# Kernel optimization log

Hardware: AMD Instinct MI355X
Metric: run time of the kernel (lower is better)

The kernel has to match this reference:

```python
import jax, jax.numpy as jnp
import numpy as np

D_MODEL = 256
N_HEADS = 8
KEY_DIM = 256  # keras code passes key_dim=d_model
DFF = 1024
B, T, S = 8, 1024, 1024
LN_EPS = 1e-3  # keras LayerNormalization default epsilon
NEG = -1e9


def _mha(q_in, kv_in, Wq, bq, Wk, bk, Wv, bv, Wo, bo, causal):
    # q/k/v: [b, t, n, h]
    q = jnp.einsum('btd,dnh->btnh', q_in, Wq) + bq
    k = jnp.einsum('bsd,dnh->bsnh', kv_in, Wk) + bk
    v = jnp.einsum('bsd,dnh->bsnh', kv_in, Wv) + bv
    scale = 1.0 / jnp.sqrt(jnp.asarray(KEY_DIM, q.dtype))
    scores = jnp.einsum('btnh,bsnh->bnts', q * scale, k)  # [b,n,t,s]
    if causal:
        mask = jnp.tril(jnp.ones((q_in.shape[1], kv_in.shape[1]), dtype=bool))
        scores = jnp.where(mask, scores, NEG)
    attn = jax.nn.softmax(scores, axis=-1)
    out = jnp.einsum('bnts,bsnh->btnh', attn, v)
    return jnp.einsum('btnh,nhd->btd', out, Wo) + bo, attn


def _layernorm(x, gamma, beta):
    mu = jnp.mean(x, axis=-1, keepdims=True)
    var = jnp.var(x, axis=-1, keepdims=True)
    return (x - mu) * jax.lax.rsqrt(var + LN_EPS) * gamma + beta


def setup_inputs() -> dict:
    key = jax.random.key(0)
    ks = jax.random.split(key, 24)
    s = 0.02
    def n(k, shape):
        return jax.random.normal(k, shape, dtype=jnp.float32) * s
    inp = {
        'x': jax.random.normal(ks[0], (B, T, D_MODEL), dtype=jnp.float32),
        'context': jax.random.normal(ks[1], (B, S, D_MODEL), dtype=jnp.float32),
        # causal self-attention MHA params
        'Wq1': n(ks[2], (D_MODEL, N_HEADS, KEY_DIM)), 'bq1': jnp.zeros((N_HEADS, KEY_DIM), jnp.float32),
        'Wk1': n(ks[3], (D_MODEL, N_HEADS, KEY_DIM)), 'bk1': jnp.zeros((N_HEADS, KEY_DIM), jnp.float32),
        'Wv1': n(ks[4], (D_MODEL, N_HEADS, KEY_DIM)), 'bv1': jnp.zeros((N_HEADS, KEY_DIM), jnp.float32),
        'Wo1': n(ks[5], (N_HEADS, KEY_DIM, D_MODEL)), 'bo1': jnp.zeros((D_MODEL,), jnp.float32),
        'g1': jnp.ones((D_MODEL,), jnp.float32), 'be1': jnp.zeros((D_MODEL,), jnp.float32),
        # cross-attention MHA params
        'Wq2': n(ks[6], (D_MODEL, N_HEADS, KEY_DIM)), 'bq2': jnp.zeros((N_HEADS, KEY_DIM), jnp.float32),
        'Wk2': n(ks[7], (D_MODEL, N_HEADS, KEY_DIM)), 'bk2': jnp.zeros((N_HEADS, KEY_DIM), jnp.float32),
        'Wv2': n(ks[8], (D_MODEL, N_HEADS, KEY_DIM)), 'bv2': jnp.zeros((N_HEADS, KEY_DIM), jnp.float32),
        'Wo2': n(ks[9], (N_HEADS, KEY_DIM, D_MODEL)), 'bo2': jnp.zeros((D_MODEL,), jnp.float32),
        'g2': jnp.ones((D_MODEL,), jnp.float32), 'be2': jnp.zeros((D_MODEL,), jnp.float32),
        # FFN params
        'W1': n(ks[10], (D_MODEL, DFF)), 'b1': jnp.zeros((DFF,), jnp.float32),
        'W2': n(ks[11], (DFF, D_MODEL)), 'b2': jnp.zeros((D_MODEL,), jnp.float32),
        'g3': jnp.ones((D_MODEL,), jnp.float32), 'be3': jnp.zeros((D_MODEL,), jnp.float32),
    }
    return inp


def reference(x, context,
              Wq1, bq1, Wk1, bk1, Wv1, bv1, Wo1, bo1, g1, be1,
              Wq2, bq2, Wk2, bk2, Wv2, bv2, Wo2, bo2, g2, be2,
              W1, b1, W2, b2, g3, be3):
    # causal self-attention + add&norm
    attn_out, _ = _mha(x, x, Wq1, bq1, Wk1, bk1, Wv1, bv1, Wo1, bo1, causal=True)
    x = _layernorm(x + attn_out, g1, be1)
    # cross-attention + add&norm
    attn_out, _ = _mha(x, context, Wq2, bq2, Wk2, bk2, Wv2, bv2, Wo2, bo2, causal=False)
    x = _layernorm(x + attn_out, g2, be2)
    # FFN (dropout is identity at inference) + add&norm
    h = jax.nn.relu(jnp.einsum('btd,df->btf', x, W1) + b1)
    ff = jnp.einsum('btf,fd->btd', h, W2) + b2
    x = _layernorm(x + ff, g3, be3)
    return x
```

## Files before the change

kernel.cpp:

```cpp
#include <hip/hip_runtime.h>
#include <hip/hip_bf16.h>
#include <math.h>

#define BATCH   8
#define SEQ     1024
#define DMODEL  256
#define NHEADS  8
#define HDIM    256
#define NQKV    2048
#define DFF     1024
#define MROWS   (BATCH*SEQ)
#define LN_EPS  1e-3f
#define ATT_SCALE 0.0625f

typedef unsigned int  uint;
typedef unsigned short ushort;
typedef __attribute__((ext_vector_type(8))) __bf16 bf16x8;
typedef __attribute__((ext_vector_type(4))) float   f32x4;
typedef __attribute__((ext_vector_type(4))) ushort  ushort4v;

__device__ __forceinline__ float b2f(ushort h) {
    union { uint u; float f; } v; v.u = ((uint)h) << 16; return v.f;
}
__device__ __forceinline__ ushort f2b(float f) {
    union { float f; uint u; } v; v.f = f;
    return (ushort)((v.u + 0x7FFFu + ((v.u >> 16) & 1u)) >> 16);
}
__device__ __forceinline__ uint pk2(float a, float b) {
    return (uint)f2b(a) | ((uint)f2b(b) << 16);
}

template<int EPI, int OUTBF>
__global__ __launch_bounds__(256, 2)
void gemm_bf16(const ushort* __restrict__ A, const ushort* __restrict__ Bt,
               const float* __restrict__ bias, const float* __restrict__ resid,
               void* __restrict__ Cv, int K, int lda, int ldc)
{
    __shared__ ushort As[128 * 64];
    __shared__ ushort Bs[128 * 64];
    const int t  = threadIdx.x;
    const int l  = t & 63;
    const int w  = t >> 6;
    const int wm = w >> 1, wn = w & 1;
    const int m0 = blockIdx.y * 128, n0 = blockIdx.x * 128;
    const int lg = l >> 4, lr = l & 15;

    f32x4 acc[4][4];
    #pragma unroll
    for (int i = 0; i < 4; i++)
        #pragma unroll
        for (int j = 0; j < 4; j++)
            acc[i][j] = (f32x4){0.f, 0.f, 0.f, 0.f};

    for (int k0 = 0; k0 < K; k0 += 64) {
        uint4 av[4], bv[4];
        #pragma unroll
        for (int j = 0; j < 4; j++) {
            const int chunk = t + j * 256;
            const int row   = chunk >> 3;
            const int ce    = (chunk & 7) * 8;
            av[j] = *(const uint4*)&A [(size_t)(m0 + row) * lda + k0 + ce];
            bv[j] = *(const uint4*)&Bt[(size_t)(n0 + row) * K   + k0 + ce];
        }
        __syncthreads();
        #pragma unroll
        for (int j = 0; j < 4; j++) {
            const int chunk = t + j * 256;
            const int row   = chunk >> 3;
            const int woff  = (chunk * 16) ^ ((row & 7) << 4);
            *(uint4*)((char*)As + woff) = av[j];
            *(uint4*)((char*)Bs + woff) = bv[j];
        }
        __syncthreads();
        #pragma unroll
        for (int c = 0; c < 2; c++) {
            bf16x8 af[4], bf[4];
            #pragma unroll
            for (int i = 0; i < 4; i++) {
                const int rowA = wm * 64 + i * 16 + lr;
                const int offA = (rowA * 128 + c * 64 + lg * 16) ^ ((rowA & 7) << 4);
                af[i] = *(const bf16x8*)((const char*)As + offA);
                const int rowB = wn * 64 + i * 16 + lr;
                const int offB = (rowB * 128 + c * 64 + lg * 16) ^ ((rowB & 7) << 4);
                bf[i] = *(const bf16x8*)((const char*)Bs + offB);
            }
            #pragma unroll
            for (int mi = 0; mi < 4; mi++)
                #pragma unroll
                for (int ni = 0; ni < 4; ni++)
                    acc[mi][ni] = __builtin_amdgcn_mfma_f32_16x16x32_bf16(
                        af[mi], bf[ni], acc[mi][ni], 0, 0, 0);
        }
    }

    #pragma unroll
    for (int ni = 0; ni < 4; ni++) {
        const int col = n0 + wn * 64 + ni * 16 + lr;
        const float bb = bias[col];
        #pragma unroll
        for (int mi = 0; mi < 4; mi++) {
            #pragma unroll
            for (int r = 0; r < 4; r++) {
                const int row = m0 + wm * 64 + mi * 16 + lg * 4 + r;
                float v = acc[mi][ni][r] + bb;
                if (EPI == 1) v = fmaxf(v, 0.f);
                if (EPI == 2) v += resid[(size_t)row * ldc + col];
                if (OUTBF) ((ushort*)Cv)[(size_t)row * ldc + col] = f2b(v);
                else       ((float*) Cv)[(size_t)row * ldc + col] = v;
            }
        }
    }
}

__global__ __launch_bounds__(256)
void vtrans(const ushort* __restrict__ V, ushort* __restrict__ Vt)
{
    __shared__ ushort tl[64][72];
    const int s0 = blockIdx.x * 64;
    const int d0 = blockIdx.y * 64;
    const int bh = blockIdx.z;
    const int b  = bh >> 3, h = bh & 7;
    const int t  = threadIdx.x;
    #pragma unroll
    for (int j = 0; j < 2; j++) {
        const int chunk = t + j * 256;
        const int row = chunk >> 3, c8 = (chunk & 7) * 8;
        *(uint4*)&tl[row][c8] =
            *(const uint4*)&V[((size_t)(b * SEQ + s0 + row)) * NQKV + h * HDIM + d0 + c8];
    }
    __syncthreads();
    #pragma unroll
    for (int j = 0; j < 2; j++) {
        const int chunk = t + j * 256;
        const int dr = chunk >> 3, s8 = (chunk & 7) * 8;
        ushort tmp[8] __attribute__((aligned(16)));
        #pragma unroll
        for (int i = 0; i < 8; i++) tmp[i] = tl[s8 + i][dr];
        *(uint4*)&Vt[((size_t)(bh * HDIM + d0 + dr)) * SEQ + s0 + s8] = *(const uint4*)tmp;
    }
}

template<bool CAUSAL>
__global__ __launch_bounds__(256, 1)
void attn_mfma(const ushort* __restrict__ Q, const ushort* __restrict__ K,
               const ushort* __restrict__ Vt, ushort* __restrict__ O)
{
    __shared__ __align__(16) char lds[37888];

    const int t  = threadIdx.x;
    const int w  = t >> 6, l = t & 63;
    const int lg = l >> 4, lr = l & 15;
    const int orig = blockIdx.x + (blockIdx.y << 4) + (blockIdx.z << 7);
    const int lin  = ((orig & 7) << 7) + (orig >> 3);
    const int qt0  = (lin & 15) << 6;
    const int h    = (lin >> 4) & 7;
    const int b    = lin >> 7;

    const size_t qgbase = ((size_t)(b * SEQ + qt0)) * NQKV + (size_t)h * HDIM;
    #pragma unroll
    for (int j = 0; j < 8; j++) {
        const int chunk = t + j * 256;
        const int row = chunk >> 5, slot = chunk & 31;
        const uint4 v = *(const uint4*)&Q[qgbase + (size_t)row * NQKV + slot * 8];
        *(uint4*)(lds + row * 512 + ((slot * 16) ^ ((row & 7) << 4))) = v;
    }

    const size_t kgbase = (size_t)b * SEQ * NQKV + (size_t)h * HDIM;
    const size_t vgbase = ((size_t)(b * NHEADS + h)) * HDIM * SEQ;
    const int ntiles = CAUSAL ? (qt0 / 32 + 2) : (SEQ / 32);

    uint4 kv[4], vv[4];
    #pragma unroll
    for (int j = 0; j < 4; j++) {
        const int chunk = t + j * 256;
        const int krow = chunk >> 5, kslot = chunk & 31;
        kv[j] = *(const uint4*)&K[kgbase + (size_t)krow * NQKV + kslot * 8];
        const int vrow = chunk >> 2, vslot = chunk & 3;
        vv[j] = *(const uint4*)&Vt[vgbase + (size_t)vrow * SEQ + vslot * 8];
    }

    __syncthreads();
    bf16x8 qa[8];
    {
        const int qrow = w * 16 + lr;
        const int sw = (qrow & 7) << 4;
        #pragma unroll
        for (int ks = 0; ks < 8; ks++)
            qa[ks] = *(const bf16x8*)(lds + qrow * 512 + ((lg * 16 + ks * 64) ^ sw));
    }

    f32x4 oacc[16];
    #pragma unroll
    for (int i = 0; i < 16; i++) oacc[i] = (f32x4){0.f, 0.f, 0.f, 0.f};
    float m_[4], l_[4];
    #pragma unroll
    for (int r = 0; r < 4; r++) { m_[r] = -INFINITY; l_[r] = 0.f; }

    ushort* Pw = (ushort*)(lds + 32768 + w * 1280);

    for (int tile = 0; tile < ntiles; tile++) {
        const int s0 = tile * 32;
        __syncthreads();
        #pragma unroll
        for (int j = 0; j < 4; j++) {
            const int chunk = t + j * 256;
            const int krow = chunk >> 5, kslot = chunk & 31;
            *(uint4*)(lds + krow * 512 + ((kslot * 16) ^ ((krow & 7) << 4))) = kv[j];
            const int vrow = chunk >> 2, vslot = chunk & 3;
            *(uint4*)(lds + 16384 + vrow * 64 + ((vslot * 16) ^ ((vrow & 3) << 4))) = vv[j];
        }
        __syncthreads();

        if (tile + 1 < ntiles) {
            const int s0n = s0 + 32;
            #pragma unroll
            for (int j = 0; j < 4; j++) {
                const int chunk = t + j * 256;
                const int krow = chunk >> 5, kslot = chunk & 31;
                kv[j] = *(const uint4*)&K[kgbase + (size_t)(s0n + krow) * NQKV + kslot * 8];
                const int vrow = chunk >> 2, vslot = chunk & 3;
                vv[j] = *(const uint4*)&Vt[vgbase + (size_t)vrow * SEQ + s0n + vslot * 8];
            }
        }

        f32x4 sacc[2];
        sacc[0] = (f32x4){0.f, 0.f, 0.f, 0.f};
        sacc[1] = (f32x4){0.f, 0.f, 0.f, 0.f};
        #pragma unroll
        for (int ks = 0; ks < 8; ks++) {
            #pragma unroll
            for (int st = 0; st < 2; st++) {
                const int srow = st * 16 + lr;
                const bf16x8 kb = *(const bf16x8*)(lds + srow * 512 +
                                   ((lg * 16 + ks * 64) ^ ((srow & 7) << 4)));
                sacc[st] = __builtin_amdgcn_mfma_f32_16x16x32_bf16(qa[ks], kb, sacc[st], 0, 0, 0);
            }
        }

        const bool maskq = CAUSAL && (s0 + 31 > qt0 + w * 16);
        float e0[4], e1[4], corr[4];
        #pragma unroll
        for (int r = 0; r < 4; r++) {
            float p0 = sacc[0][r] * ATT_SCALE;
            float p1 = sacc[1][r] * ATT_SCALE;
            if (maskq) {
                const int qg = qt0 + w * 16 + lg * 4 + r;
                if (s0 + lr > qg)      p0 = -1e9f;
                if (s0 + 16 + lr > qg) p1 = -1e9f;
            }
            float mx = fmaxf(p0, p1);
            mx = fmaxf(mx, __shfl_xor(mx, 1));
            mx = fmaxf(mx, __shfl_xor(mx, 2));
            mx = fmaxf(mx, __shfl_xor(mx, 4));
            mx = fmaxf(mx, __shfl_xor(mx, 8));
            const float newm = fmaxf(m_[r], mx);
            corr[r] = __expf(m_[r] - newm);
            m_[r] = newm;
            e0[r] = __expf(p0 - newm);
            e1[r] = __expf(p1 - newm);
            float es = e0[r] + e1[r];
            es += __shfl_xor(es, 1);
            es += __shfl_xor(es, 2);
            es += __shfl_xor(es, 4);
            es += __shfl_xor(es, 8);
            l_[r] = l_[r] * corr[r] + es;
        }
        #pragma unroll
        for (int r = 0; r < 4; r++) {
            Pw[(lg * 4 + r) * 40 + lr]      = f2b(e0[r]);
            Pw[(lg * 4 + r) * 40 + 16 + lr] = f2b(e1[r]);
        }
        #pragma unroll
        for (int dt = 0; dt < 16; dt++) {
            oacc[dt][0] *= corr[0]; oacc[dt][1] *= corr[1];
            oacc[dt][2] *= corr[2]; oacc[dt][3] *= corr[3];
        }

        const bf16x8 pa = *(const bf16x8*)((const char*)Pw + lr * 80 + lg * 16);
        #pragma unroll
        for (int dt = 0; dt < 16; dt++) {
            const int vrow = dt * 16 + lr;
            const bf16x8 vb = *(const bf16x8*)(lds + 16384 + vrow * 64 +
                               ((lg * 16) ^ ((vrow & 3) << 4)));
            oacc[dt] = __builtin_amdgcn_mfma_f32_16x16x32_bf16(pa, vb, oacc[dt], 0, 0, 0);
        }
    }

    float inv[4];
    #pragma unroll
    for (int r = 0; r < 4; r++) inv[r] = 1.f / l_[r];
    const size_t obase = ((size_t)(b * SEQ + qt0 + w * 16)) * NQKV + (size_t)h * HDIM;
    #pragma unroll
    for (int dt = 0; dt < 16; dt++) {
        #pragma unroll
        for (int r = 0; r < 4; r++) {
            O[obase + (size_t)(lg * 4 + r) * NQKV + dt * 16 + lr] =
                f2b(oacc[dt][r] * inv[r]);
        }
    }
}

__global__ __launch_bounds__(256)
void ln_f32(const float* __restrict__ X, const float* __restrict__ gamma,
            const float* __restrict__ beta, float* __restrict__ Y,
            ushort* __restrict__ Yb)
{
    const int lane = threadIdx.x & 63;
    const int row  = blockIdx.x * 4 + (threadIdx.x >> 6);
    const float4 v = *(const float4*)&X[(size_t)row * DMODEL + lane * 4];
    float s = v.x + v.y + v.z + v.w;
    #pragma unroll
    for (int o = 1; o < 64; o <<= 1) s += __shfl_xor(s, o);
    const float mu = s * (1.f / 256.f);
    const float dx = v.x - mu, dy = v.y - mu, dz = v.z - mu, dw = v.w - mu;
    float ss = dx*dx + dy*dy + dz*dz + dw*dw;
    #pragma unroll
    for (int o = 1; o < 64; o <<= 1) ss += __shfl_xor(ss, o);
    const float rstd = rsqrtf(ss * (1.f / 256.f) + LN_EPS);
    const float4 gv = *(const float4*)&gamma[lane * 4];
    const float4 bv = *(const float4*)&beta[lane * 4];
    float4 out;
    out.x = dx * rstd * gv.x + bv.x;
    out.y = dy * rstd * gv.y + bv.y;
    out.z = dz * rstd * gv.z + bv.z;
    out.w = dw * rstd * gv.w + bv.w;
    *(float4*)&Y[(size_t)row * DMODEL + lane * 4] = out;
    if (Yb) {
        uint2 p; p.x = pk2(out.x, out.y); p.y = pk2(out.z, out.w);
        *(uint2*)&Yb[(size_t)row * DMODEL + lane * 4] = p;
    }
}

__global__ __launch_bounds__(256)
void cast_f2b(const float* __restrict__ X, ushort* __restrict__ Y, int n8)
{
    const int i = blockIdx.x * 256 + threadIdx.x;
    if (i < n8) {
        const float4 a = *(const float4*)&X[(size_t)i * 8];
        const float4 b = *(const float4*)&X[(size_t)i * 8 + 4];
        uint4 o;
        o.x = pk2(a.x, a.y); o.y = pk2(a.z, a.w);
        o.z = pk2(b.x, b.y); o.w = pk2(b.z, b.w);
        *(uint4*)&Y[(size_t)i * 8] = o;
    }
}

__global__ __launch_bounds__(256)
void castT_f2b(const float* __restrict__ W, ushort* __restrict__ Wt, int Kd, int Nd)
{
    __shared__ float tile[32][33];
    const int k0 = blockIdx.y * 32, n0 = blockIdx.x * 32;
    const int r  = threadIdx.x >> 3;
    const int c4 = (threadIdx.x & 7) * 4;
    const float4 v = *(const float4*)&W[(size_t)(k0 + r) * Nd + n0 + c4];
    tile[r][c4+0] = v.x; tile[r][c4+1] = v.y; tile[r][c4+2] = v.z; tile[r][c4+3] = v.w;
    __syncthreads();
    ushort4v ov = { f2b(tile[c4+0][r]), f2b(tile[c4+1][r]),
                    f2b(tile[c4+2][r]), f2b(tile[c4+3][r]) };
    *(ushort4v*)&Wt[(size_t)(n0 + r) * Kd + k0 + c4] = ov;
}

extern "C" void kernel_launch(void* const* d_in, const int* in_sizes, int n_in,
                              void* d_out, int out_size, void* d_ws, size_t ws_size,
                              hipStream_t stream)
{
    const float* x    = (const float*)d_in[0];
    const float* ctx  = (const float*)d_in[1];
    const float* Wq1  = (const float*)d_in[2];
    const float* bq1  = (const float*)d_in[3];
    const float* Wk1  = (const float*)d_in[4];
    const float* bk1  = (const float*)d_in[5];
    const float* Wv1  = (const float*)d_in[6];
    const float* bv1  = (const float*)d_in[7];
    const float* Wo1  = (const float*)d_in[8];
    const float* bo1  = (const float*)d_in[9];
    const float* g1   = (const float*)d_in[10];
    const float* be1  = (const float*)d_in[11];
    const float* Wq2  = (const float*)d_in[12];
    const float* bq2  = (const float*)d_in[13];
    const float* Wk2  = (const float*)d_in[14];
    const float* bk2  = (const float*)d_in[15];
    const float* Wv2  = (const float*)d_in[16];
    const float* bv2  = (const float*)d_in[17];
    const float* Wo2  = (const float*)d_in[18];
    const float* bo2  = (const float*)d_in[19];
    const float* g2   = (const float*)d_in[20];
    const float* be2  = (const float*)d_in[21];
    const float* W1   = (const float*)d_in[22];
    const float* b1   = (const float*)d_in[23];
    const float* W2   = (const float*)d_in[24];
    const float* b2   = (const float*)d_in[25];
    const float* g3   = (const float*)d_in[26];
    const float* be3  = (const float*)d_in[27];
    (void)in_sizes; (void)n_in; (void)out_size; (void)ws_size;

    char* base = (char*)d_ws;
    const size_t MB1 = 1024 * 1024;
    ushort* Qb   = (ushort*)(base + 0 * MB1);
    ushort* Kb   = (ushort*)(base + 32 * MB1);
    ushort* Vb   = (ushort*)(base + 64 * MB1);
    float*  Yf   = (float*) (base + 96 * MB1);
    float*  X1f  = (float*) (base + 104 * MB1);
    float*  X2f  = (float*) (base + 112 * MB1);
    ushort* xb   = (ushort*)(base + 120 * MB1);
    ushort* ctxb = (ushort*)(base + 124 * MB1);
    ushort* X1b  = (ushort*)(base + 128 * MB1);
    ushort* X2b  = (ushort*)(base + 132 * MB1);
    ushort* wq1t = (ushort*)(base + 136 * MB1);
    ushort* wk1t = (ushort*)(base + 137 * MB1);
    ushort* wv1t = (ushort*)(base + 138 * MB1);
    ushort* wo1t = (ushort*)(base + 139 * MB1);
    ushort* wq2t = (ushort*)(base + 140 * MB1);
    ushort* wk2t = (ushort*)(base + 141 * MB1);
    ushort* wv2t = (ushort*)(base + 142 * MB1);
    ushort* wo2t = (ushort*)(base + 143 * MB1);
    ushort* w1t  = (ushort*)(base + 144 * MB1);
    ushort* w2t  = (ushort*)(base + 144 * MB1 + 512 * 1024);
    ushort* Hb   = (ushort*)(base + 145 * MB1);
    ushort* Vtg  = (ushort*)(base + 161 * MB1);

    const dim3 blk(256);
    const dim3 gQKV(NQKV/128, MROWS/128);
    const dim3 gOut(DMODEL/128, MROWS/128);
    const dim3 gF1(DFF/128, MROWS/128);
    const dim3 gAttn(SEQ/64, NHEADS, BATCH);
    const dim3 gVT(SEQ/64, HDIM/64, BATCH*NHEADS);
    const dim3 gLN(MROWS/4);

    cast_f2b<<<dim3((MROWS*DMODEL/8 + 255)/256), blk, 0, stream>>>(x,   xb,   MROWS*DMODEL/8);
    cast_f2b<<<dim3((MROWS*DMODEL/8 + 255)/256), blk, 0, stream>>>(ctx, ctxb, MROWS*DMODEL/8);
    castT_f2b<<<dim3(NQKV/32, DMODEL/32), blk, 0, stream>>>(Wq1, wq1t, DMODEL, NQKV);
    castT_f2b<<<dim3(NQKV/32, DMODEL/32), blk, 0, stream>>>(Wk1, wk1t, DMODEL, NQKV);
    castT_f2b<<<dim3(NQKV/32, DMODEL/32), blk, 0, stream>>>(Wv1, wv1t, DMODEL, NQKV);
    castT_f2b<<<dim3(DMODEL/32, NQKV/32), blk, 0, stream>>>(Wo1, wo1t, NQKV, DMODEL);
    castT_f2b<<<dim3(NQKV/32, DMODEL/32), blk, 0, stream>>>(Wq2, wq2t, DMODEL, NQKV);
    castT_f2b<<<dim3(NQKV/32, DMODEL/32), blk, 0, stream>>>(Wk2, wk2t, DMODEL, NQKV);
    castT_f2b<<<dim3(NQKV/32, DMODEL/32), blk, 0, stream>>>(Wv2, wv2t, DMODEL, NQKV);
    castT_f2b<<<dim3(DMODEL/32, NQKV/32), blk, 0, stream>>>(Wo2, wo2t, NQKV, DMODEL);
    castT_f2b<<<dim3(DFF/32, DMODEL/32), blk, 0, stream>>>(W1, w1t, DMODEL, DFF);
    castT_f2b<<<dim3(DMODEL/32, DFF/32), blk, 0, stream>>>(W2, w2t, DFF, DMODEL);

    gemm_bf16<0,1><<<gQKV, blk, 0, stream>>>(xb, wq1t, bq1, nullptr, Qb, DMODEL, DMODEL, NQKV);
    gemm_bf16<0,1><<<gQKV, blk, 0, stream>>>(xb, wk1t, bk1, nullptr, Kb, DMODEL, DMODEL, NQKV);
    gemm_bf16<0,1><<<gQKV, blk, 0, stream>>>(xb, wv1t, bv1, nullptr, Vb, DMODEL, DMODEL, NQKV);
    vtrans<<<gVT, blk, 0, stream>>>(Vb, Vtg);
    attn_mfma<true><<<gAttn, blk, 0, stream>>>(Qb, Kb, Vtg, Qb);
    gemm_bf16<2,0><<<gOut, blk, 0, stream>>>(Qb, wo1t, bo1, x, Yf, NQKV, NQKV, DMODEL);
    ln_f32<<<gLN, blk, 0, stream>>>(Yf, g1, be1, X1f, X1b);
    gemm_bf16<0,1><<<gQKV, blk, 0, stream>>>(X1b,  wq2t, bq2, nullptr, Qb, DMODEL, DMODEL, NQKV);
    gemm_bf16<0,1><<<gQKV, blk, 0, stream>>>(ctxb, wk2t, bk2, nullptr, Kb, DMODEL, DMODEL, NQKV);
    gemm_bf16<0,1><<<gQKV, blk, 0, stream>>>(ctxb, wv2t, bv2, nullptr, Vb, DMODEL, DMODEL, NQKV);
    vtrans<<<gVT, blk, 0, stream>>>(Vb, Vtg);
    attn_mfma<false><<<gAttn, blk, 0, stream>>>(Qb, Kb, Vtg, Qb);
    gemm_bf16<2,0><<<gOut, blk, 0, stream>>>(Qb, wo2t, bo2, X1f, Yf, NQKV, NQKV, DMODEL);
    ln_f32<<<gLN, blk, 0, stream>>>(Yf, g2, be2, X2f, X2b);
    gemm_bf16<1,1><<<gF1,  blk, 0, stream>>>(X2b, w1t, b1, nullptr, Hb, DMODEL, DMODEL, DFF);
    gemm_bf16<2,0><<<gOut, blk, 0, stream>>>(Hb, w2t, b2, X2f, Yf, DFF, DFF, DMODEL);
    ln_f32<<<gLN, blk, 0, stream>>>(Yf, g3, be3, (float*)d_out, nullptr);
}
```

Measured before the change: 1.359 ms.

## Double-buffer K/V tiles in attention with lazy softmax rescale and MFMA priority

Attention K/V tiles now go into two LDS buffers, so the next tile is written while the current one is consumed, which cuts the loop from two barriers per tile to one. Softmax skips the max reduction and the output rescale when every lane's new scores stay within a threshold of the running max, and the row-sum reduction is deferred to the end. s_setprio is raised around the MFMA loops. LDS use grows to about 70KB, and the lazy-max path relies on exp staying bounded, which trades some numerical headroom for less work.

Measured after the change: 1.407 ms. 3.5% more time.

```diff
diff --git a/kernel.cpp b/kernel.cpp
--- a/kernel.cpp
+++ b/kernel.cpp
@@ -145,7 +145,7 @@
 void attn_mfma(const ushort* __restrict__ Q, const ushort* __restrict__ K,
                const ushort* __restrict__ Vt, ushort* __restrict__ O)
 {
-    __shared__ __align__(16) char lds[37888];
+    __shared__ __align__(16) char lds[70656];
 
     const int t  = threadIdx.x;
     const int w  = t >> 6, l = t & 63;
@@ -169,14 +169,24 @@
     const size_t vgbase = ((size_t)(b * NHEADS + h)) * HDIM * SEQ;
     const int ntiles = CAUSAL ? (qt0 / 32 + 2) : (SEQ / 32);
 
-    uint4 kv[4], vv[4];
+    int kwoff[4], vwoff[4];
+    size_t kgoff[4], vgoff[4];
     #pragma unroll
     for (int j = 0; j < 4; j++) {
         const int chunk = t + j * 256;
         const int krow = chunk >> 5, kslot = chunk & 31;
-        kv[j] = *(const uint4*)&K[kgbase + (size_t)krow * NQKV + kslot * 8];
+        kwoff[j] = krow * 512 + ((kslot * 16) ^ ((krow & 7) << 4));
+        kgoff[j] = (size_t)krow * NQKV + kslot * 8;
         const int vrow = chunk >> 2, vslot = chunk & 3;
-        vv[j] = *(const uint4*)&Vt[vgbase + (size_t)vrow * SEQ + vslot * 8];
+        vwoff[j] = vrow * 64 + ((vslot * 16) ^ ((vrow & 3) << 4));
+        vgoff[j] = (size_t)vrow * SEQ + vslot * 8;
+    }
+
+    uint4 kv[4], vv[4];
+    #pragma unroll
+    for (int j = 0; j < 4; j++) {
+        kv[j] = *(const uint4*)&K[kgbase + kgoff[j]];
+        vv[j] = *(const uint4*)&Vt[vgbase + vgoff[j]];
     }
 
     __syncthreads();
@@ -188,6 +198,21 @@
         for (int ks = 0; ks < 8; ks++)
             qa[ks] = *(const bf16x8*)(lds + qrow * 512 + ((lg * 16 + ks * 64) ^ sw));
     }
+    __syncthreads();
+
+    #pragma unroll
+    for (int j = 0; j < 4; j++) {
+        *(uint4*)(lds + kwoff[j])         = kv[j];
+        *(uint4*)(lds + 32768 + vwoff[j]) = vv[j];
+    }
+    if (ntiles > 1) {
+        #pragma unroll
+        for (int j = 0; j < 4; j++) {
+            kv[j] = *(const uint4*)&K[kgbase + (size_t)32 * NQKV + kgoff[j]];
+            vv[j] = *(const uint4*)&Vt[vgbase + 32 + vgoff[j]];
+        }
+    }
+    __syncthreads();
 
     f32x4 oacc[16];
     #pragma unroll
@@ -196,49 +221,31 @@
     #pragma unroll
     for (int r = 0; r < 4; r++) { m_[r] = -INFINITY; l_[r] = 0.f; }
 
-    ushort* Pw = (ushort*)(lds + 32768 + w * 1280);
+    ushort* Pw = (ushort*)(lds + 65536 + w * 1280);
+    int curoff = 0;
 
     for (int tile = 0; tile < ntiles; tile++) {
         const int s0 = tile * 32;
-        __syncthreads();
-        #pragma unroll
-        for (int j = 0; j < 4; j++) {
-            const int chunk = t + j * 256;
-            const int krow = chunk >> 5, kslot = chunk & 31;
-            *(uint4*)(lds + krow * 512 + ((kslot * 16) ^ ((krow & 7) << 4))) = kv[j];
-            const int vrow = chunk >> 2, vslot = chunk & 3;
-            *(uint4*)(lds + 16384 + vrow * 64 + ((vslot * 16) ^ ((vrow & 3) << 4))) = vv[j];
-        }
-        __syncthreads();
-
-        if (tile + 1 < ntiles) {
-            const int s0n = s0 + 32;
-            #pragma unroll
-            for (int j = 0; j < 4; j++) {
-                const int chunk = t + j * 256;
-                const int krow = chunk >> 5, kslot = chunk & 31;
-                kv[j] = *(const uint4*)&K[kgbase + (size_t)(s0n + krow) * NQKV + kslot * 8];
-                const int vrow = chunk >> 2, vslot = chunk & 3;
-                vv[j] = *(const uint4*)&Vt[vgbase + (size_t)vrow * SEQ + s0n + vslot * 8];
-            }
-        }
 
         f32x4 sacc[2];
         sacc[0] = (f32x4){0.f, 0.f, 0.f, 0.f};
         sacc[1] = (f32x4){0.f, 0.f, 0.f, 0.f};
+        __builtin_amdgcn_s_setprio(1);
         #pragma unroll
         for (int ks = 0; ks < 8; ks++) {
             #pragma unroll
             for (int st = 0; st < 2; st++) {
                 const int srow = st * 16 + lr;
-                const bf16x8 kb = *(const bf16x8*)(lds + srow * 512 +
+                const bf16x8 kb = *(const bf16x8*)(lds + curoff + srow * 512 +
                                    ((lg * 16 + ks * 64) ^ ((srow & 7) << 4)));
                 sacc[st] = __builtin_amdgcn_mfma_f32_16x16x32_bf16(qa[ks], kb, sacc[st], 0, 0, 0);
             }
         }
+        __builtin_amdgcn_s_setprio(0);
 
         const bool maskq = CAUSAL && (s0 + 31 > qt0 + w * 16);
-        float e0[4], e1[4], corr[4];
+        float p0s[4], p1s[4];
+        bool ok = true;
         #pragma unroll
         for (int r = 0; r < 4; r++) {
             float p0 = sacc[0][r] * ATT_SCALE;
@@ -248,47 +255,84 @@
                 if (s0 + lr > qg)      p0 = -1e9f;
                 if (s0 + 16 + lr > qg) p1 = -1e9f;
             }
-            float mx = fmaxf(p0, p1);
-            mx = fmaxf(mx, __shfl_xor(mx, 1));
-            mx = fmaxf(mx, __shfl_xor(mx, 2));
-            mx = fmaxf(mx, __shfl_xor(mx, 4));
-            mx = fmaxf(mx, __shfl_xor(mx, 8));
-            const float newm = fmaxf(m_[r], mx);
-            corr[r] = __expf(m_[r] - newm);
-            m_[r] = newm;
-            e0[r] = __expf(p0 - newm);
-            e1[r] = __expf(p1 - newm);
-            float es = e0[r] + e1[r];
-            es += __shfl_xor(es, 1);
-            es += __shfl_xor(es, 2);
-            es += __shfl_xor(es, 4);
-            es += __shfl_xor(es, 8);
-            l_[r] = l_[r] * corr[r] + es;
-        }
-        #pragma unroll
-        for (int r = 0; r < 4; r++) {
-            Pw[(lg * 4 + r) * 40 + lr]      = f2b(e0[r]);
-            Pw[(lg * 4 + r) * 40 + 16 + lr] = f2b(e1[r]);
-        }
-        #pragma unroll
-        for (int dt = 0; dt < 16; dt++) {
-            oacc[dt][0] *= corr[0]; oacc[dt][1] *= corr[1];
-            oacc[dt][2] *= corr[2]; oacc[dt][3] *= corr[3];
+            p0s[r] = p0; p1s[r] = p1;
+            ok &= (fmaxf(p0, p1) <= m_[r] + 8.f);
+        }
+        if (__all((int)ok)) {
+            #pragma unroll
+            for (int r = 0; r < 4; r++) {
+                const float e0 = __expf(p0s[r] - m_[r]);
+                const float e1 = __expf(p1s[r] - m_[r]);
+                l_[r] += e0 + e1;
+                Pw[(lg * 4 + r) * 40 + lr]      = f2b(e0);
+                Pw[(lg * 4 + r) * 40 + 16 + lr] = f2b(e1);
+            }
+        } else {
+            float corr[4];
+            #pragma unroll
+            for (int r = 0; r < 4; r++) {
+                float mx = fmaxf(p0s[r], p1s[r]);
+                mx = fmaxf(mx, __shfl_xor(mx, 1));
+                mx = fmaxf(mx, __shfl_xor(mx, 2));
+                mx = fmaxf(mx, __shfl_xor(mx, 4));
+                mx = fmaxf(mx, __shfl_xor(mx, 8));
+                const float newm = fmaxf(m_[r], mx);
+                corr[r] = __expf(m_[r] - newm);
+                m_[r] = newm;
+                const float e0 = __expf(p0s[r] - newm);
+                const float e1 = __expf(p1s[r] - newm);
+                l_[r] = l_[r] * corr[r] + e0 + e1;
+                Pw[(lg * 4 + r) * 40 + lr]      = f2b(e0);
+                Pw[(lg * 4 + r) * 40 + 16 + lr] = f2b(e1);
+            }
+            #pragma unroll
+            for (int dt = 0; dt < 16; dt++) {
+                oacc[dt][0] *= corr[0]; oacc[dt][1] *= corr[1];
+                oacc[dt][2] *= corr[2]; oacc[dt][3] *= corr[3];
+            }
         }
 
         const bf16x8 pa = *(const bf16x8*)((const char*)Pw + lr * 80 + lg * 16);
+        __builtin_amdgcn_s_setprio(1);
         #pragma unroll
         for (int dt = 0; dt < 16; dt++) {
             const int vrow = dt * 16 + lr;
-            const bf16x8 vb = *(const bf16x8*)(lds + 16384 + vrow * 64 +
+            const bf16x8 vb = *(const bf16x8*)(lds + 32768 + curoff + vrow * 64 +
                                ((lg * 16) ^ ((vrow & 3) << 4)));
             oacc[dt] = __builtin_amdgcn_mfma_f32_16x16x32_bf16(pa, vb, oacc[dt], 0, 0, 0);
         }
+        __builtin_amdgcn_s_setprio(0);
+
+        if (tile + 1 < ntiles) {
+            const int noff = curoff ^ 16384;
+            #pragma unroll
+            for (int j = 0; j < 4; j++) {
+                *(uint4*)(lds + noff + kwoff[j])         = kv[j];
+                *(uint4*)(lds + 32768 + noff + vwoff[j]) = vv[j];
+            }
+            if (tile + 2 < ntiles) {
+                const int s0n = s0 + 64;
+                #pragma unroll
+                for (int j = 0; j < 4; j++) {
+                    kv[j] = *(const uint4*)&K[kgbase + (size_t)s0n * NQKV + kgoff[j]];
+                    vv[j] = *(const uint4*)&Vt[vgbase + s0n + vgoff[j]];
+                }
+            }
+        }
+        __syncthreads();
+        curoff ^= 16384;
     }
 
     float inv[4];
     #pragma unroll
-    for (int r = 0; r < 4; r++) inv[r] = 1.f / l_[r];
+    for (int r = 0; r < 4; r++) {
+        float ls = l_[r];
+        ls += __shfl_xor(ls, 1);
+        ls += __shfl_xor(ls, 2);
+        ls += __shfl_xor(ls, 4);
+        ls += __shfl_xor(ls, 8);
+        inv[r] = 1.f / ls;
+    }
     const size_t obase = ((size_t)(b * SEQ + qt0 + w * 16)) * NQKV + (size_t)h * HDIM;
     #pragma unroll
     for (int dt = 0; dt < 16; dt++) {
```

## Add lazy softmax rescaling, MFMA priority hints and higher occupancy to attention

Applied to the files above, without the earlier changes.

The online-softmax loop now skips the row-max shuffle reduction and the rescaling of the output accumulators whenever every new score in the wave stays within 8 of the running max. The row-sum is kept per lane and reduced once with shuffles at the end, instead of once per tile. s_setprio is raised around both MFMA loops, and the launch bound goes from 1 to 4 blocks per CU so more waves can overlap. The tighter register budget may cause spills, and four blocks per CU must fit in LDS.

New measurement: 2.658 ms. 1.96x slower.

```diff
diff --git a/kernel.cpp b/kernel.cpp
--- a/kernel.cpp
+++ b/kernel.cpp
@@ -141,7 +141,7 @@
 }
 
 template<bool CAUSAL>
-__global__ __launch_bounds__(256, 1)
+__global__ __launch_bounds__(256, 4)
 void attn_mfma(const ushort* __restrict__ Q, const ushort* __restrict__ K,
                const ushort* __restrict__ Vt, ushort* __restrict__ O)
 {
@@ -226,6 +226,7 @@
         f32x4 sacc[2];
         sacc[0] = (f32x4){0.f, 0.f, 0.f, 0.f};
         sacc[1] = (f32x4){0.f, 0.f, 0.f, 0.f};
+        __builtin_amdgcn_s_setprio(1);
         #pragma unroll
         for (int ks = 0; ks < 8; ks++) {
             #pragma unroll
@@ -236,9 +237,9 @@
                 sacc[st] = __builtin_amdgcn_mfma_f32_16x16x32_bf16(qa[ks], kb, sacc[st], 0, 0, 0);
             }
         }
+        __builtin_amdgcn_s_setprio(0);
 
         const bool maskq = CAUSAL && (s0 + 31 > qt0 + w * 16);
-        float e0[4], e1[4], corr[4];
         #pragma unroll
         for (int r = 0; r < 4; r++) {
             float p0 = sacc[0][r] * ATT_SCALE;
@@ -248,35 +249,48 @@
                 if (s0 + lr > qg)      p0 = -1e9f;
                 if (s0 + 16 + lr > qg) p1 = -1e9f;
             }
-            float mx = fmaxf(p0, p1);
-            mx = fmaxf(mx, __shfl_xor(mx, 1));
-            mx = fmaxf(mx, __shfl_xor(mx, 2));
-            mx = fmaxf(mx, __shfl_xor(mx, 4));
-            mx = fmaxf(mx, __shfl_xor(mx, 8));
-            const float newm = fmaxf(m_[r], mx);
-            corr[r] = __expf(m_[r] - newm);
-            m_[r] = newm;
-            e0[r] = __expf(p0 - newm);
-            e1[r] = __expf(p1 - newm);
-            float es = e0[r] + e1[r];
-            es += __shfl_xor(es, 1);
-            es += __shfl_xor(es, 2);
-            es += __shfl_xor(es, 4);
-            es += __shfl_xor(es, 8);
-            l_[r] = l_[r] * corr[r] + es;
-        }
-        #pragma unroll
-        for (int r = 0; r < 4; r++) {
-            Pw[(lg * 4 + r) * 40 + lr]      = f2b(e0[r]);
-            Pw[(lg * 4 + r) * 40 + 16 + lr] = f2b(e1[r]);
-        }
-        #pragma unroll
-        for (int dt = 0; dt < 16; dt++) {
-            oacc[dt][0] *= corr[0]; oacc[dt][1] *= corr[1];
-            oacc[dt][2] *= corr[2]; oacc[dt][3] *= corr[3];
+            sacc[0][r] = p0; sacc[1][r] = p1;
+        }
+        bool ok = true;
+        #pragma unroll
+        for (int r = 0; r < 4; r++)
+            ok &= (fmaxf(sacc[0][r], sacc[1][r]) <= m_[r] + 8.f);
+        if (__all((int)ok)) {
+            #pragma unroll
+            for (int r = 0; r < 4; r++) {
+                const float e0 = __expf(sacc[0][r] - m_[r]);
+                const float e1 = __expf(sacc[1][r] - m_[r]);
+                l_[r] += e0 + e1;
+                Pw[(lg * 4 + r) * 40 + lr]      = f2b(e0);
+                Pw[(lg * 4 + r) * 40 + 16 + lr] = f2b(e1);
+            }
+        } else {
+            float corr[4];
+            #pragma unroll
+            for (int r = 0; r < 4; r++) {
+                float mx = fmaxf(sacc[0][r], sacc[1][r]);
+                mx = fmaxf(mx, __shfl_xor(mx, 1));
+                mx = fmaxf(mx, __shfl_xor(mx, 2));
+                mx = fmaxf(mx, __shfl_xor(mx, 4));
+                mx = fmaxf(mx, __shfl_xor(mx, 8));
+                const float newm = fmaxf(m_[r], mx);
+                corr[r] = __expf(m_[r] - newm);
+                m_[r] = newm;
+                const float e0 = __expf(sacc[0][r] - newm);
+                const float e1 = __expf(sacc[1][r] - newm);
+                l_[r] = l_[r] * corr[r] + e0 + e1;
+                Pw[(lg * 4 + r) * 40 + lr]      = f2b(e0);
+                Pw[(lg * 4 + r) * 40 + 16 + lr] = f2b(e1);
+            }
+            #pragma unroll
+            for (int dt = 0; dt < 16; dt++) {
+                oacc[dt][0] *= corr[0]; oacc[dt][1] *= corr[1];
+                oacc[dt][2] *= corr[2]; oacc[dt][3] *= corr[3];
+            }
         }
 
         const bf16x8 pa = *(const bf16x8*)((const char*)Pw + lr * 80 + lg * 16);
+        __builtin_amdgcn_s_setprio(1);
         #pragma unroll
         for (int dt = 0; dt < 16; dt++) {
             const int vrow = dt * 16 + lr;
@@ -284,11 +298,19 @@
                                ((lg * 16) ^ ((vrow & 3) << 4)));
             oacc[dt] = __builtin_amdgcn_mfma_f32_16x16x32_bf16(pa, vb, oacc[dt], 0, 0, 0);
         }
+        __builtin_amdgcn_s_setprio(0);
     }
 
     float inv[4];
     #pragma unroll
-    for (int r = 0; r < 4; r++) inv[r] = 1.f / l_[r];
+    for (int r = 0; r < 4; r++) {
+        float ls = l_[r];
+        ls += __shfl_xor(ls, 1);
+        ls += __shfl_xor(ls, 2);
+        ls += __shfl_xor(ls, 4);
+        ls += __shfl_xor(ls, 8);
+        inv[r] = 1.f / ls;
+    }
     const size_t obase = ((size_t)(b * SEQ + qt0 + w * 16)) * NQKV + (size_t)h * HDIM;
     #pragma unroll
     for (int dt = 0; dt < 16; dt++) {
```
